# Performance work log

Measured on AMD Instinct MI355X. Metric: run time of the kernel, lower is better.

## Reference

```python
import jax, jax.numpy as jnp
import numpy as np

B, T, V, C = 4, 2048, 1024, 256
NB_L, NB_M, NB_H = 16, 32, 64


def _band_w(basis, coeffs, soft):
    # basis: (V, 2*nb), coeffs: (C, 2*nb) -> w: (V, C)
    w = basis @ coeffs.T
    return jax.nn.softmax(w, axis=0) if soft else w


def _rms_norm(x):
    eps = jnp.asarray(jnp.finfo(x.dtype).eps, x.dtype)
    return x * jax.lax.rsqrt(jnp.mean(jnp.square(x), axis=-1, keepdims=True) + eps)


def _retrieve(x, basis, qc, kc, vc, decay_logit):
    # x: (B,T,V) -> (B,T,C); decay-weighted dense T x T retrieval
    q = x @ _band_w(basis, qc, True)
    k = x @ _band_w(basis, kc, True)
    v = x @ _band_w(basis, vc, True)
    scores = jnp.einsum('btc,bsc->bts', q, k)
    decay = jax.nn.sigmoid(decay_logit)
    pos = jnp.arange(T)
    diff = pos[None, :] - pos[:, None]  # diff[i,j] = j - i (as in torch code)
    dw = (decay ** jnp.maximum(diff - 1, 0).astype(x.dtype)) * (diff > 0).astype(x.dtype)
    return jnp.einsum('bts,bsc->btc', scores * dw[None], v)


def _project(r, basis, oc, out_scale):
    return jnp.einsum('btc,vc->btv', r, basis @ oc.T) * out_scale


def _transform(x, basis, read_c, mix, bias):
    z = x @ _band_w(basis, read_c, True)
    return jax.nn.gelu(z @ mix + bias, approximate=False)


def _write_back(h, basis, write_c, out_scale):
    return jnp.einsum('btc,vc->btv', h, basis @ write_c.T) * out_scale


def setup_inputs() -> dict:
    key = jax.random.key(0)
    ks = iter(jax.random.split(key, 48))
    s = 0.02

    def rn(shape, scale=s):
        return jax.random.normal(next(ks), shape, dtype=jnp.float32) * scale

    d = {
        'x': jax.random.normal(next(ks), (B, T, V), dtype=jnp.float32),
        'basis_low': jax.random.normal(next(ks), (V, 2 * NB_L), dtype=jnp.float32),
        'basis_mid': jax.random.normal(next(ks), (V, 2 * NB_M), dtype=jnp.float32),
        'basis_high': jax.random.normal(next(ks), (V, 2 * NB_H), dtype=jnp.float32),
    }
    for pre, nb, dec in (('slow', NB_L, 4.0), ('fast', NB_H, 2.0)):
        for nm in ('q', 'k', 'v', 'o'):
            d[f'{pre}_{nm}'] = rn((C, 2 * nb))
        d[f'{pre}_decay'] = jnp.asarray(dec, jnp.float32)
        d[f'{pre}_scale'] = jnp.asarray(0.1, jnp.float32)
    for pre, nb in (('low', NB_L), ('mid', NB_M), ('high', NB_H)):
        d[f'{pre}_read'] = rn((C, 2 * nb))
        d[f'{pre}_write'] = rn((C, 2 * nb))
        d[f'{pre}_mix'] = rn((C, C))
        d[f'{pre}_bias'] = jnp.zeros((C,), jnp.float32)
        d[f'{pre}_oscale'] = jnp.asarray(0.1, jnp.float32)
    d['tg_w'] = rn((C, C)); d['tg_b'] = jnp.zeros((C,), jnp.float32)
    d['alpha_w'] = rn((C, C)); d['alpha_b'] = jnp.zeros((C,), jnp.float32)
    for nm in ('mem_slow_scale', 'mem_fast_scale', 'op_low_scale', 'op_mid_scale', 'op_high_scale'):
        d[nm] = jnp.ones((1,), jnp.float32)
    return d


def reference(x, basis_low, basis_mid, basis_high,
              slow_q, slow_k, slow_v, slow_o, slow_decay, slow_scale,
              fast_q, fast_k, fast_v, fast_o, fast_decay, fast_scale,
              low_read, low_write, low_mix, low_bias, low_oscale,
              mid_read, mid_write, mid_mix, mid_bias, mid_oscale,
              high_read, high_write, high_mix, high_bias, high_oscale,
              tg_w, tg_b, alpha_w, alpha_b,
              mem_slow_scale, mem_fast_scale, op_low_scale, op_mid_scale, op_high_scale):
    # Phase 1: temporal mixing
    xn = _rms_norm(x)
    r_slow = _retrieve(xn, basis_low, slow_q, slow_k, slow_v, slow_decay)
    r_fast = _retrieve(xn, basis_high, fast_q, fast_k, fast_v, fast_decay)
    tg = jax.nn.sigmoid(r_slow @ tg_w + tg_b)
    r_fast = tg * r_fast
    x = x + (_project(r_slow, basis_low, slow_o, slow_scale) * mem_slow_scale
             + _project(r_fast, basis_high, fast_o, fast_scale) * mem_fast_scale)
    # Phase 2: band processing
    xn = _rms_norm(x)
    h_low = _transform(xn, basis_low, low_read, low_mix, low_bias)
    h_mid = _transform(xn, basis_mid, mid_read, mid_mix, mid_bias)
    h_high = _transform(xn, basis_high, high_read, high_mix, high_bias)
    ag = jax.nn.sigmoid(h_low @ alpha_w + alpha_b)
    h_high = ag * h_high
    x = x + (_write_back(h_low, basis_low, low_write, low_oscale) * op_low_scale
             + _write_back(h_mid, basis_mid, mid_write, mid_oscale) * op_mid_scale
             + _write_back(h_high, basis_high, high_write, high_oscale) * op_high_scale)
    return x
```

## Files before the change

### kernel.cpp

```cpp
#include <hip/hip_runtime.h>
#include <math.h>

#define BB 4
#define TT 2048
#define VV 1024
#define CC 256
#define MR (BB*TT)

using short8  = __attribute__((ext_vector_type(8))) short;
using ushort8 = __attribute__((ext_vector_type(8))) unsigned short;
using f32x4   = __attribute__((ext_vector_type(4))) float;

__device__ __forceinline__ float bs2f(unsigned short s) {
    return __uint_as_float(((unsigned int)s) << 16);
}
__device__ __forceinline__ unsigned short f2bs(float f) {
    unsigned int u = __float_as_uint(f);
    u += 0x7fffu + ((u >> 16) & 1u);
    return (unsigned short)(u >> 16);
}
__device__ __forceinline__ void gl_lds16(const void* g, void* l) {
    __builtin_amdgcn_global_load_lds(
        (const __attribute__((address_space(1))) unsigned int*)g,
        (__attribute__((address_space(3))) unsigned int*)l, 16, 0, 0);
}
__device__ __forceinline__ float sigm(float x) { return 1.f / (1.f + expf(-x)); }
__device__ __forceinline__ float erf_f(float x) {
    float ax = fabsf(x);
    float t = 1.f / (1.f + 0.3275911f * ax);
    float p = t * (0.254829592f + t * (-0.284496736f + t * (1.421413741f +
              t * (-1.453152027f + t * 1.061405429f))));
    float e = 1.f - p * expf(-ax * ax);
    return copysignf(e, x);
}

struct CastJob { const float* src; unsigned short* dst; int n; };
struct CastArgs { CastJob j[17]; };

__global__ void cast_bf16_multi(CastArgs a) {
    CastJob jb = a.j[blockIdx.x];
    int off = (blockIdx.y * 256 + threadIdx.x) * 8;
    if (off + 8 > jb.n) return;
    float4 v0 = *reinterpret_cast<const float4*>(jb.src + off);
    float4 v1 = *reinterpret_cast<const float4*>(jb.src + off + 4);
    ushort8 u;
    u[0] = f2bs(v0.x); u[1] = f2bs(v0.y); u[2] = f2bs(v0.z); u[3] = f2bs(v0.w);
    u[4] = f2bs(v1.x); u[5] = f2bs(v1.y); u[6] = f2bs(v1.z); u[7] = f2bs(v1.w);
    *reinterpret_cast<ushort8*>(jb.dst + off) = u;
}

__global__ void softmax_rows(unsigned short* __restrict__ w) {
    int row = blockIdx.x * 4 + (threadIdx.x >> 6);
    int lane = threadIdx.x & 63;
    ushort4* rp = reinterpret_cast<ushort4*>(w + (size_t)row * 1024);
    float v[16];
    #pragma unroll
    for (int i = 0; i < 4; ++i) {
        ushort4 u = rp[lane + i * 64];
        v[i*4+0] = bs2f(u.x); v[i*4+1] = bs2f(u.y);
        v[i*4+2] = bs2f(u.z); v[i*4+3] = bs2f(u.w);
    }
    float m = v[0];
    #pragma unroll
    for (int i = 1; i < 16; ++i) m = fmaxf(m, v[i]);
    #pragma unroll
    for (int o = 32; o > 0; o >>= 1) m = fmaxf(m, __shfl_xor(m, o));
    float s = 0.f;
    #pragma unroll
    for (int i = 0; i < 16; ++i) { v[i] = expf(v[i] - m); s += v[i]; }
    #pragma unroll
    for (int o = 32; o > 0; o >>= 1) s += __shfl_xor(s, o);
    float inv = 1.f / s;
    #pragma unroll
    for (int i = 0; i < 4; ++i) {
        ushort4 u;
        u.x = f2bs(v[i*4+0] * inv); u.y = f2bs(v[i*4+1] * inv);
        u.z = f2bs(v[i*4+2] * inv); u.w = f2bs(v[i*4+3] * inv);
        rp[lane + i * 64] = u;
    }
}

__global__ void prep_T5(const float* s0, const float* s1, const float* s2,
                        const float* s3, const float* s4,
                        unsigned short* d0, unsigned short* d1, unsigned short* d2,
                        unsigned short* d3, unsigned short* d4) {
    int y = blockIdx.y;
    const float* W = y == 0 ? s0 : y == 1 ? s1 : y == 2 ? s2 : y == 3 ? s3 : s4;
    unsigned short* WT = y == 0 ? d0 : y == 1 ? d1 : y == 2 ? d2 : y == 3 ? d3 : d4;
    int n = blockIdx.x, k = threadIdx.x;
    WT[(size_t)n * 256 + k] = f2bs(W[(size_t)k * 256 + n]);
}

__global__ void rmsnorm_k(const float* __restrict__ x, unsigned short* __restrict__ xn) {
    int row = blockIdx.x * 4 + (threadIdx.x >> 6);
    int lane = threadIdx.x & 63;
    const float4* src = reinterpret_cast<const float4*>(x + (size_t)row * VV);
    float4 v[4];
    float s = 0.f;
    #pragma unroll
    for (int i = 0; i < 4; ++i) {
        v[i] = src[lane + i * 64];
        s += v[i].x*v[i].x + v[i].y*v[i].y + v[i].z*v[i].z + v[i].w*v[i].w;
    }
    #pragma unroll
    for (int o = 32; o > 0; o >>= 1) s += __shfl_xor(s, o);
    float r = rsqrtf(s * (1.f / VV) + 1.1920929e-7f);
    ushort4* dst = reinterpret_cast<ushort4*>(xn + (size_t)row * VV);
    #pragma unroll
    for (int i = 0; i < 4; ++i) {
        ushort4 u;
        u.x = f2bs(v[i].x * r); u.y = f2bs(v[i].y * r);
        u.z = f2bs(v[i].z * r); u.w = f2bs(v[i].w * r);
        dst[lane + i * 64] = u;
    }
}

__global__ void transpose4_k(const unsigned short* __restrict__ qkv,
                             unsigned short* __restrict__ vt_s,
                             unsigned short* __restrict__ vt_f,
                             unsigned short* __restrict__ kts_s,
                             unsigned short* __restrict__ kts_f,
                             const float* __restrict__ dls,
                             const float* __restrict__ dlf) {
    __shared__ unsigned short tile[32][33];
    int z = blockIdx.z, b = z & 3, which = z >> 2;
    int srcoff = which == 0 ? 512 : which == 1 ? 1280 : which == 2 ? 256 : 1024;
    unsigned short* dst = which == 0 ? vt_s : which == 1 ? vt_f : which == 2 ? kts_s : kts_f;
    float l2d = 0.f;
    if (which == 2) l2d = log2f(sigm(dls[0]));
    if (which == 3) l2d = log2f(sigm(dlf[0]));
    int t0 = blockIdx.x * 32, c0 = blockIdx.y * 32;
    int tx = threadIdx.x & 31, ty = threadIdx.x >> 5;
    const unsigned short* src = qkv + srcoff;
    #pragma unroll
    for (int i = 0; i < 4; ++i) {
        int r = ty + i * 8;
        tile[r][tx] = src[(size_t)(b * TT + t0 + r) * 1536 + c0 + tx];
    }
    __syncthreads();
    float w = (which >= 2) ? exp2f(l2d * (float)((t0 + tx) & 127)) : 1.f;
    #pragma unroll
    for (int i = 0; i < 4; ++i) {
        int r = ty + i * 8;
        dst[((size_t)b * CC + c0 + r) * TT + t0 + tx] = f2bs(bs2f(tile[tx][r]) * w);
    }
}

__device__ __forceinline__ void gemm64_core(
    const unsigned short* A, int lda, const unsigned short* Bt, int ldb,
    int K, int m0, int n0, short8* As, short8* Bs, f32x4 (&acc)[2][2]) {
    const int tid = threadIdx.x;
    const int lane = tid & 63, wid = tid >> 6;
    const int wm = wid >> 1, wn = wid & 1;
    const int lrow = tid >> 2, lch = tid & 3;
    const int sws = lch ^ ((lrow >> 1) & 3);
    const unsigned short* ag = A + (size_t)(m0 + lrow) * lda + lch * 8;
    const unsigned short* bg = Bt + (size_t)(n0 + lrow) * ldb + lch * 8;
    #pragma unroll
    for (int i = 0; i < 2; ++i)
        #pragma unroll
        for (int j = 0; j < 2; ++j) acc[i][j] = {0.f, 0.f, 0.f, 0.f};
    const int g = lane >> 4;
    const int ra0 = wm * 32 + (lane & 15);
    const int rb0 = wn * 32 + (lane & 15);
    for (int k0 = 0; k0 < K; k0 += 32) {
        As[lrow * 4 + sws] = *reinterpret_cast<const short8*>(ag + k0);
        Bs[lrow * 4 + sws] = *reinterpret_cast<const short8*>(bg + k0);
        __syncthreads();
        short8 af[2], bf[2];
        #pragma unroll
        for (int i = 0; i < 2; ++i) {
            int ra = ra0 + i * 16;
            af[i] = As[ra * 4 + (g ^ ((ra >> 1) & 3))];
            int rb = rb0 + i * 16;
            bf[i] = Bs[rb * 4 + (g ^ ((rb >> 1) & 3))];
        }
        #pragma unroll
        for (int i = 0; i < 2; ++i)
            #pragma unroll
            for (int j = 0; j < 2; ++j)
                acc[i][j] = __builtin_amdgcn_mfma_f32_16x16x32_bf16(af[i], bf[j], acc[i][j], 0, 0, 0);
        __syncthreads();
    }
}

#define EPI_LOOP(MV, NV, VV_, BODY)                                            \
    {   const int lane_ = threadIdx.x & 63, wid_ = threadIdx.x >> 6;           \
        const int wm_ = wid_ >> 1, wn_ = wid_ & 1;                             \
        _Pragma("unroll")                                                      \
        for (int i_ = 0; i_ < 2; ++i_)                                         \
        { _Pragma("unroll")                                                    \
          for (int j_ = 0; j_ < 2; ++j_)                                       \
          { _Pragma("unroll")                                                  \
            for (int r_ = 0; r_ < 4; ++r_)                                     \
            { int MV = m0 + wm_ * 32 + i_ * 16 + (lane_ >> 4) * 4 + r_;        \
              int NV = n0 + wn_ * 32 + j_ * 16 + (lane_ & 15);                 \
              float VV_ = acc[i_][j_][r_];                                     \
              BODY } } } }

struct MJob {
    const unsigned short* A; const unsigned short* Bt; unsigned short* outb;
    const float* s1; const float* s2;
    int lda, ldb, K, ldo, gx, nblk;
};
struct MJobs5 { MJob j[5]; };

template<int EPI>
__global__ __launch_bounds__(256)
void gemm_multi_k(MJobs5 js) {
    int bid = blockIdx.x, ji = 0, base = 0;
    while (bid >= base + js.j[ji].nblk) { base += js.j[ji].nblk; ++ji; }
    MJob jb = js.j[ji];
    int rem = bid - base;
    int m0 = (rem / jb.gx) * 64, n0 = (rem % jb.gx) * 64;
    __shared__ short8 As[256], Bs[256];
    f32x4 acc[2][2];
    gemm64_core(jb.A, jb.lda, jb.Bt, jb.ldb, jb.K, m0, n0, As, Bs, acc);
    float sc = 1.f;
    if constexpr (EPI == 4) sc = jb.s1[0] * jb.s2[0];
    EPI_LOOP(m, n, v, { jb.outb[(size_t)m * jb.ldo + n] = f2bs(v * sc); })
}

__global__ __launch_bounds__(256)
void sig_k(const unsigned short* A, int lda, const unsigned short* Bt,
           const float* bias, const unsigned short* aux, int ldaux,
           unsigned short* outb, int ldo, int coloff) {
    int m0 = blockIdx.y * 64, n0 = blockIdx.x * 64;
    __shared__ short8 As[256], Bs[256];
    f32x4 acc[2][2];
    gemm64_core(A, lda, Bt, 256, 256, m0, n0, As, Bs, acc);
    EPI_LOOP(m, n, v, {
        float s = sigm(v + bias[n]);
        float a = bs2f(aux[(size_t)m * ldaux + n]);
        outb[(size_t)m * ldo + coloff + n] = f2bs(s * a);
    })
}

__global__ __launch_bounds__(256)
void gelu3_k(const unsigned short* zbuf, const unsigned short* WT_mix,
             const float* lb, const float* mb, const float* hb,
             unsigned short* hcat, unsigned short* hhigh) {
    int zi = blockIdx.z;
    const unsigned short* A = zbuf + zi * 256;
    const unsigned short* Bt = WT_mix + (size_t)zi * 65536;
    const float* bias = zi == 0 ? lb : zi == 1 ? mb : hb;
    unsigned short* outb = zi == 2 ? hhigh : hcat;
    int ldo = zi == 2 ? 256 : 768;
    int coloff = zi == 1 ? 256 : 0;
    int m0 = blockIdx.y * 64, n0 = blockIdx.x * 64;
    __shared__ short8 As[256], Bs[256];
    f32x4 acc[2][2];
    gemm64_core(A, 768, Bt, 256, 256, m0, n0, As, Bs, acc);
    EPI_LOOP(m, n, v, {
        float z = v + bias[n];
        float h = 0.5f * z * (1.f + erf_f(z * 0.70710678118654752f));
        outb[(size_t)m * ldo + coloff + n] = f2bs(h);
    })
}

__global__ __launch_bounds__(256)
void inter_k(const unsigned short* qkv,
             const unsigned short* ST_s, const unsigned short* ST_f,
             const float* dls, const float* dlf,
             unsigned short* rcat, unsigned short* rfast) {
    int zz = blockIdx.z;
    int sel = zz >= 60, z2 = sel ? zz - 60 : zz;
    int zb = z2 / 15, zp = z2 % 15;
    const unsigned short* A = qkv + (sel ? 768 : 0) + (size_t)(zb * TT + zp * 128) * 1536;
    const unsigned short* Bt = (sel ? ST_f : ST_s) + (size_t)z2 * 65536;
    unsigned short* outb = sel ? rfast : rcat;
    int ldo = sel ? 256 : 512;
    float l2d = log2f(sigm(sel ? dlf[0] : dls[0]));
    int m0 = blockIdx.y * 64, n0 = blockIdx.x * 64;
    __shared__ short8 As[256], Bs[256];
    f32x4 acc[2][2];
    gemm64_core(A, 1536, Bt, 256, 256, m0, n0, As, Bs, acc);
    EPI_LOOP(m, n, v, {
        float rs = exp2f(l2d * (float)(127 - m));
        size_t idx = (size_t)(zb * TT + zp * 128 + m) * ldo + n;
        outb[idx] = f2bs(bs2f(outb[idx]) + v * rs);
    })
}

struct EpiP {
    float* outf; const float* addf;
    unsigned short* outb; int ldo;
    const unsigned short* A2; const unsigned short* B2;
    float* outf2;
};

template<int EPI, int BATCH>
__global__ __launch_bounds__(256)
void gemm128_k(const unsigned short* __restrict__ A, int lda,
               const unsigned short* __restrict__ Bt, int ldb, int K, EpiP ep) {
    __shared__ short8 As[2][512], Bs[2][512];
    const int tid = threadIdx.x;
    const int lane = tid & 63, wid = tid >> 6;
    const int wm = wid >> 1, wn = wid & 1;

    int sel = 0, z2v = 0;
    if constexpr (BATCH == 1) {
        int zz = blockIdx.z; sel = zz >> 6; z2v = zz & 63;
        int zb = z2v >> 4, zp = z2v & 15;
        if (sel) { A = ep.A2; Bt = ep.B2; }
        A  += (size_t)(zb * CC) * lda + zp * 128;
        Bt += (size_t)(zb * CC) * ldb + zp * 128;
    }

    int lin = blockIdx.y * gridDim.x + blockIdx.x;
    int ngw = gridDim.x * gridDim.y;
    int sw = lin;
    if (!(ngw & 7)) sw = (lin & 7) * (ngw >> 3) + (lin >> 3);
    const int m0 = (sw / gridDim.x) * 128, n0 = (sw % gridDim.x) * 128;

    const int srow = lane >> 2, schk = (lane & 3) ^ ((srow >> 1) & 3);
    const unsigned short* ga = A + (size_t)(m0 + wid * 32 + srow) * lda + schk * 8;
    const unsigned short* gb = Bt + (size_t)(n0 + wid * 32 + srow) * ldb + schk * 8;

    const int fr = lane & 15, fg = lane >> 4;

    f32x4 acc[4][4];
    #pragma unroll
    for (int i = 0; i < 4; ++i)
        #pragma unroll
        for (int j = 0; j < 4; ++j) acc[i][j] = {0.f, 0.f, 0.f, 0.f};

    auto stage = [&](int buf, int k0) {
        short8* lA = &As[buf][(wid * 32) * 4];
        short8* lB = &Bs[buf][(wid * 32) * 4];
        gl_lds16(ga + k0, lA);
        gl_lds16(ga + (size_t)16 * lda + k0, lA + 64);
        gl_lds16(gb + k0, lB);
        gl_lds16(gb + (size_t)16 * ldb + k0, lB + 64);
    };

    stage(0, 0);
    int cur = 0;
    for (int k0 = 0; k0 < K; k0 += 32) {
        if (k0 + 32 < K) {
            stage(cur ^ 1, k0 + 32);
            asm volatile("s_waitcnt vmcnt(4)" ::: "memory");
        } else {
            asm volatile("s_waitcnt vmcnt(0)" ::: "memory");
        }
        __builtin_amdgcn_s_barrier();
        __builtin_amdgcn_sched_barrier(0);
        short8 af[4], bf[4];
        #pragma unroll
        for (int i = 0; i < 4; ++i) {
            int ra = wm * 64 + i * 16 + fr;
            af[i] = As[cur][ra * 4 + (fg ^ ((ra >> 1) & 3))];
            int rb = wn * 64 + i * 16 + fr;
            bf[i] = Bs[cur][rb * 4 + (fg ^ ((rb >> 1) & 3))];
        }
        #pragma unroll
        for (int i = 0; i < 4; ++i)
            #pragma unroll
            for (int j = 0; j < 4; ++j)
                acc[i][j] = __builtin_amdgcn_mfma_f32_16x16x32_bf16(af[i], bf[j], acc[i][j], 0, 0, 0);
        __builtin_amdgcn_sched_barrier(0);
        __builtin_amdgcn_s_barrier();
        cur ^= 1;
    }

    float* gout = nullptr;
    if constexpr (EPI == 5) gout = (sel ? ep.outf2 : ep.outf) + (size_t)z2v * 65536;

    #pragma unroll
    for (int i = 0; i < 4; ++i) {
        #pragma unroll
        for (int j = 0; j < 4; ++j) {
            #pragma unroll
            for (int r = 0; r < 4; ++r) {
                int m = m0 + wm * 64 + i * 16 + fg * 4 + r;
                int n = n0 + wn * 64 + j * 16 + fr;
                float v = acc[i][j][r];
                if constexpr (EPI == 0) {
                    ep.outb[(size_t)m * ep.ldo + n] = f2bs(v);
                } else if constexpr (EPI == 3) {
                    size_t idx = (size_t)m * ep.ldo + n;
                    ep.outf[idx] = ep.addf[idx] + v;
                } else {
                    gout[(size_t)m * 256 + n] = v;
                }
            }
        }
    }
}

__global__ __launch_bounds__(256)
void attn_k(const unsigned short* __restrict__ qkv,
            const unsigned short* __restrict__ vt_s,
            const unsigned short* __restrict__ vt_f,
            const float* __restrict__ dls, const float* __restrict__ dlf,
            unsigned short* __restrict__ rcat, unsigned short* __restrict__ rfast) {
    int y = blockIdx.y;
    int qoff = y ? 768 : 0, koff = y ? 1024 : 256;
    const unsigned short* vt = y ? vt_f : vt_s;
    unsigned short* rout = y ? rfast : rcat;
    int ldr = y ? 256 : 512;
    float l2d = log2f(sigm(y ? dlf[0] : dls[0]));

    int blk = blockIdx.x;
    int b = blk >> 7;
    int t0 = (blk & 127) << 4;
    int tid = threadIdx.x;
    int lane = tid & 63, wid = tid >> 6;

    __shared__ short8 Pl[4][64];
    __shared__ float  red[16][260];

    short8 qf[8];
    const size_t rowq = (size_t)(b * TT + t0 + (lane & 15)) * 1536 + qoff + (lane >> 4) * 8;
    #pragma unroll
    for (int ch = 0; ch < 8; ++ch)
        qf[ch] = *reinterpret_cast<const short8*>(qkv + rowq + ch * 32);

    f32x4 racc[16];
    #pragma unroll
    for (int i = 0; i < 16; ++i) racc[i] = {0.f, 0.f, 0.f, 0.f};

    unsigned short* pb = reinterpret_cast<unsigned short*>(&Pl[wid][0]);

    int sBeg = t0 & ~31;
    int sEnd = (t0 & ~127) + 128;
    const int tl = (lane >> 4) * 4;

    for (int s0 = sBeg + wid * 32; s0 < sEnd; s0 += 128) {
        #pragma unroll
        for (int h = 0; h < 2; ++h) {
            f32x4 sacc = {0.f, 0.f, 0.f, 0.f};
            const unsigned short* kb =
                qkv + (size_t)(b * TT + s0 + h * 16 + (lane & 15)) * 1536 + koff + (lane >> 4) * 8;
            #pragma unroll
            for (int ch = 0; ch < 8; ++ch) {
                short8 kf = *reinterpret_cast<const short8*>(kb + ch * 32);
                sacc = __builtin_amdgcn_mfma_f32_16x16x32_bf16(qf[ch], kf, sacc, 0, 0, 0);
            }
            int scol = s0 + h * 16 + (lane & 15);
            #pragma unroll
            for (int r = 0; r < 4; ++r) {
                int trow = t0 + tl + r;
                int d = scol - trow;
                float w = (d > 0) ? exp2f(l2d * (float)(d - 1)) : 0.f;
                int prow = tl + r, pcol = h * 16 + (lane & 15);
                int swp = (pcol >> 3) ^ ((prow >> 1) & 3);
                pb[(prow * 4 + swp) * 8 + (pcol & 7)] = f2bs(sacc[r] * w);
            }
        }
        asm volatile("s_waitcnt lgkmcnt(0)" ::: "memory");
        __builtin_amdgcn_sched_barrier(0);
        short8 pf;
        { int prow = lane & 15; pf = Pl[wid][prow * 4 + ((lane >> 4) ^ ((prow >> 1) & 3))]; }
        const unsigned short* vb = vt + ((size_t)b * CC + (lane & 15)) * TT + s0 + (lane >> 4) * 8;
        #pragma unroll
        for (int nt = 0; nt < 16; ++nt) {
            short8 vf = *reinterpret_cast<const short8*>(vb + (size_t)nt * 16 * TT);
            racc[nt] = __builtin_amdgcn_mfma_f32_16x16x32_bf16(pf, vf, racc[nt], 0, 0, 0);
        }
    }

    for (int w = 0; w < 4; ++w) {
        if (wid == w) {
            #pragma unroll
            for (int nt = 0; nt < 16; ++nt)
                #pragma unroll
                for (int r = 0; r < 4; ++r) {
                    int row = tl + r, col = nt * 16 + (lane & 15);
                    if (w == 0) red[row][col] = racc[nt][r];
                    else        red[row][col] += racc[nt][r];
                }
        }
        __syncthreads();
    }

    {
        int row = tid >> 4, c0 = (tid & 15) * 16;
        ushort8 lo, hi;
        #pragma unroll
        for (int j = 0; j < 8; ++j) lo[j] = f2bs(red[row][c0 + j]);
        #pragma unroll
        for (int j = 0; j < 8; ++j) hi[j] = f2bs(red[row][c0 + 8 + j]);
        unsigned short* dst = rout + (size_t)(b * TT + t0 + row) * ldr + c0;
        *reinterpret_cast<ushort8*>(dst)     = lo;
        *reinterpret_cast<ushort8*>(dst + 8) = hi;
    }
}

__global__ void scan_states2(const float* __restrict__ Gs, const float* __restrict__ Gf,
                             const float* __restrict__ dls, const float* __restrict__ dlf,
                             unsigned short* __restrict__ STs, unsigned short* __restrict__ STf) {
    int sel = blockIdx.z;
    const float* G = sel ? Gf : Gs;
    unsigned short* ST = sel ? STf : STs;
    float d = sigm(sel ? dlf[0] : dls[0]);
    int b = blockIdx.y;
    int e0 = (blockIdx.x * 256 + threadIdx.x) * 4;
    float dL = exp2f(log2f(d) * 128.f);
    float4 s = {0.f, 0.f, 0.f, 0.f};
    for (int c = 15; c >= 1; --c) {
        float4 g = *reinterpret_cast<const float4*>(G + (((size_t)(b * 16 + c)) << 16) + e0);
        s.x = g.x + dL * s.x; s.y = g.y + dL * s.y;
        s.z = g.z + dL * s.z; s.w = g.w + dL * s.w;
        ushort4 o;
        o.x = f2bs(s.x); o.y = f2bs(s.y); o.z = f2bs(s.z); o.w = f2bs(s.w);
        *reinterpret_cast<ushort4*>(ST + (((size_t)(b * 15 + c - 1)) << 16) + e0) = o;
    }
}

extern "C" void kernel_launch(void* const* d_in, const int* in_sizes, int n_in,
                              void* d_out, int out_size, void* d_ws, size_t ws_size,
                              hipStream_t stream) {
    (void)in_sizes; (void)n_in; (void)out_size; (void)ws_size;
    const float* x          = (const float*)d_in[0];
    const float* basis_low  = (const float*)d_in[1];
    const float* basis_mid  = (const float*)d_in[2];
    const float* basis_high = (const float*)d_in[3];
    const float* slow_q = (const float*)d_in[4];
    const float* slow_k = (const float*)d_in[5];
    const float* slow_v = (const float*)d_in[6];
    const float* slow_o = (const float*)d_in[7];
    const float* slow_decay = (const float*)d_in[8];
    const float* slow_scale = (const float*)d_in[9];
    const float* fast_q = (const float*)d_in[10];
    const float* fast_k = (const float*)d_in[11];
    const float* fast_v = (const float*)d_in[12];
    const float* fast_o = (const float*)d_in[13];
    const float* fast_decay = (const float*)d_in[14];
    const float* fast_scale = (const float*)d_in[15];
    const float* low_read  = (const float*)d_in[16];
    const float* low_write = (const float*)d_in[17];
    const float* low_mix   = (const float*)d_in[18];
    const float* low_bias  = (const float*)d_in[19];
    const float* low_oscale= (const float*)d_in[20];
    const float* mid_read  = (const float*)d_in[21];
    const float* mid_write = (const float*)d_in[22];
    const float* mid_mix   = (const float*)d_in[23];
    const float* mid_bias  = (const float*)d_in[24];
    const float* mid_oscale= (const float*)d_in[25];
    const float* high_read  = (const float*)d_in[26];
    const float* high_write = (const float*)d_in[27];
    const float* high_mix   = (const float*)d_in[28];
    const float* high_bias  = (const float*)d_in[29];
    const float* high_oscale= (const float*)d_in[30];
    const float* tg_w    = (const float*)d_in[31];
    const float* tg_b    = (const float*)d_in[32];
    const float* alpha_w = (const float*)d_in[33];
    const float* alpha_b = (const float*)d_in[34];
    const float* mem_slow_scale = (const float*)d_in[35];
    const float* mem_fast_scale = (const float*)d_in[36];
    const float* op_low_scale   = (const float*)d_in[37];
    const float* op_mid_scale   = (const float*)d_in[38];
    const float* op_high_scale  = (const float*)d_in[39];
    float* out = (float*)d_out;

    char* ws = (char*)d_ws;
    size_t off = 0;
    auto alloc = [&](size_t n) { char* p = ws + off; off += (n + 255) & ~(size_t)255; return p; };
    unsigned short* WT_p1   = (unsigned short*)alloc((size_t)6 * CC * VV * 2);
    unsigned short* WT_read = (unsigned short*)alloc((size_t)3 * CC * VV * 2);
    unsigned short* Wcat_o  = (unsigned short*)alloc((size_t)VV * 512 * 2);
    unsigned short* Wcat_w  = (unsigned short*)alloc((size_t)VV * 768 * 2);
    unsigned short* WT_mix  = (unsigned short*)alloc((size_t)3 * 65536 * 2);
    unsigned short* WT_tg   = (unsigned short*)alloc((size_t)65536 * 2);
    unsigned short* WT_al   = (unsigned short*)alloc((size_t)65536 * 2);
    unsigned short* bb_low  = (unsigned short*)alloc((size_t)VV * 32 * 2);
    unsigned short* bb_mid  = (unsigned short*)alloc((size_t)VV * 64 * 2);
    unsigned short* bb_high = (unsigned short*)alloc((size_t)VV * 128 * 2);
    unsigned short* cqkv_l  = (unsigned short*)alloc((size_t)768 * 32 * 2);
    unsigned short* cqkv_h  = (unsigned short*)alloc((size_t)768 * 128 * 2);
    unsigned short* crd_l   = (unsigned short*)alloc((size_t)256 * 32 * 2);
    unsigned short* crd_m   = (unsigned short*)alloc((size_t)256 * 64 * 2);
    unsigned short* crd_h   = (unsigned short*)alloc((size_t)256 * 128 * 2);
    unsigned short* cO_s    = (unsigned short*)alloc((size_t)256 * 32 * 2);
    unsigned short* cO_f    = (unsigned short*)alloc((size_t)256 * 128 * 2);
    unsigned short* cW_l    = (unsigned short*)alloc((size_t)256 * 32 * 2);
    unsigned short* cW_m    = (unsigned short*)alloc((size_t)256 * 64 * 2);
    unsigned short* cW_h    = (unsigned short*)alloc((size_t)256 * 128 * 2);
    unsigned short* xn      = (unsigned short*)alloc((size_t)MR * VV * 2);
    unsigned short* qkv     = (unsigned short*)alloc((size_t)MR * 1536 * 2);
    unsigned short* vt_s    = (unsigned short*)alloc((size_t)BB * CC * TT * 2);
    unsigned short* vt_f    = (unsigned short*)alloc((size_t)BB * CC * TT * 2);
    unsigned short* kts_s   = (unsigned short*)alloc((size_t)BB * CC * TT * 2);
    unsigned short* kts_f   = (unsigned short*)alloc((size_t)BB * CC * TT * 2);
    unsigned short* ST_s    = (unsigned short*)alloc((size_t)BB * 15 * 65536 * 2);
    unsigned short* ST_f    = (unsigned short*)alloc((size_t)BB * 15 * 65536 * 2);
    unsigned short* rcat    = (unsigned short*)alloc((size_t)MR * 512 * 2);
    unsigned short* rfast   = (unsigned short*)alloc((size_t)MR * CC * 2);
    unsigned short* hhigh   = (unsigned short*)alloc((size_t)MR * CC * 2);
    float* Gs = (float*)xn;
    float* Gf = (float*)rcat;
    unsigned short* z    = qkv;
    unsigned short* hcat = qkv + (size_t)MR * 768;

    {
        CastArgs ca;
        int i = 0;
        auto J = [&](const float* s, unsigned short* d, int n) { ca.j[i].src = s; ca.j[i].dst = d; ca.j[i].n = n; ++i; };
        J(basis_low,  bb_low,  VV * 32);
        J(basis_mid,  bb_mid,  VV * 64);
        J(basis_high, bb_high, VV * 128);
        J(slow_q, cqkv_l + 0 * 256 * 32, 256 * 32);
        J(slow_k, cqkv_l + 1 * 256 * 32, 256 * 32);
        J(slow_v, cqkv_l + 2 * 256 * 32, 256 * 32);
        J(fast_q, cqkv_h + 0 * 256 * 128, 256 * 128);
        J(fast_k, cqkv_h + 1 * 256 * 128, 256 * 128);
        J(fast_v, cqkv_h + 2 * 256 * 128, 256 * 128);
        J(low_read,  crd_l, 256 * 32);
        J(mid_read,  crd_m, 256 * 64);
        J(high_read, crd_h, 256 * 128);
        J(slow_o,    cO_s,  256 * 32);
        J(fast_o,    cO_f,  256 * 128);
        J(low_write, cW_l,  256 * 32);
        J(mid_write, cW_m,  256 * 64);
        J(high_write,cW_h,  256 * 128);
        cast_bf16_multi<<<dim3(17, 64), 256, 0, stream>>>(ca);
    }

    {
        MJobs5 js;
        auto S = [&](int i, const unsigned short* A, int lda, const unsigned short* B, int K,
                     unsigned short* o, int nb) {
            js.j[i].A = A; js.j[i].Bt = B; js.j[i].outb = o; js.j[i].s1 = nullptr; js.j[i].s2 = nullptr;
            js.j[i].lda = lda; js.j[i].ldb = K; js.j[i].K = K; js.j[i].ldo = VV; js.j[i].gx = 16; js.j[i].nblk = nb;
        };
        S(0, cqkv_l, 32,  bb_low,  32,  WT_p1,                    192);
        S(1, cqkv_h, 128, bb_high, 128, WT_p1 + (size_t)768 * VV, 192);
        S(2, crd_l,  32,  bb_low,  32,  WT_read,                   64);
        S(3, crd_m,  64,  bb_mid,  64,  WT_read + (size_t)256 * VV, 64);
        S(4, crd_h,  128, bb_high, 128, WT_read + (size_t)512 * VV, 64);
        gemm_multi_k<0><<<576, 256, 0, stream>>>(js);
    }
    softmax_rows<<<576, 256, 0, stream>>>(WT_p1);

    {
        MJobs5 js;
        auto S = [&](int i, const unsigned short* A, int lda, const unsigned short* B, int K,
                     unsigned short* o, int ldo, const float* s1, const float* s2) {
            js.j[i].A = A; js.j[i].Bt = B; js.j[i].outb = o; js.j[i].s1 = s1; js.j[i].s2 = s2;
            js.j[i].lda = lda; js.j[i].ldb = K; js.j[i].K = K; js.j[i].ldo = ldo; js.j[i].gx = 4; js.j[i].nblk = 64;
        };
        S(0, bb_low,  32,  cO_s, 32,  Wcat_o,       512, slow_scale,  mem_slow_scale);
        S(1, bb_high, 128, cO_f, 128, Wcat_o + 256, 512, fast_scale,  mem_fast_scale);
        S(2, bb_low,  32,  cW_l, 32,  Wcat_w,       768, low_oscale,  op_low_scale);
        S(3, bb_mid,  64,  cW_m, 64,  Wcat_w + 256, 768, mid_oscale,  op_mid_scale);
        S(4, bb_high, 128, cW_h, 128, Wcat_w + 512, 768, high_oscale, op_high_scale);
        gemm_multi_k<4><<<320, 256, 0, stream>>>(js);
    }

    prep_T5<<<dim3(256, 5), 256, 0, stream>>>(tg_w, alpha_w, low_mix, mid_mix, high_mix,
                                              WT_tg, WT_al, WT_mix, WT_mix + 65536, WT_mix + 131072);

    rmsnorm_k<<<MR / 4, 256, 0, stream>>>(x, xn);
    { EpiP ep{}; ep.outb = qkv; ep.ldo = 1536;
      gemm128_k<0,0><<<dim3(12, 64), 256, 0, stream>>>(xn, 1024, WT_p1, 1024, 1024, ep); }
    transpose4_k<<<dim3(64, 8, 16), 256, 0, stream>>>(qkv, vt_s, vt_f, kts_s, kts_f, slow_decay, fast_decay);
    { EpiP ep{}; ep.outf = Gs; ep.outf2 = Gf; ep.A2 = vt_f; ep.B2 = kts_f;
      gemm128_k<5,1><<<dim3(2, 2, 128), 256, 0, stream>>>(vt_s, TT, kts_s, TT, 128, ep); }
    scan_states2<<<dim3(64, 4, 2), 256, 0, stream>>>(Gs, Gf, slow_decay, fast_decay, ST_s, ST_f);
    attn_k<<<dim3(512, 2), 256, 0, stream>>>(qkv, vt_s, vt_f, slow_decay, fast_decay, rcat, rfast);
    inter_k<<<dim3(4, 2, 120), 256, 0, stream>>>(qkv, ST_s, ST_f, slow_decay, fast_decay, rcat, rfast);
    sig_k<<<dim3(4, 128), 256, 0, stream>>>(rcat, 512, WT_tg, tg_b, rfast, 256, rcat, 512, 256);
    { EpiP ep{}; ep.outf = out; ep.addf = x; ep.ldo = 1024;
      gemm128_k<3,0><<<dim3(8, 64), 256, 0, stream>>>(rcat, 512, Wcat_o, 512, 512, ep); }

    rmsnorm_k<<<MR / 4, 256, 0, stream>>>(out, xn);
    { EpiP ep{}; ep.outb = z; ep.ldo = 768;
      gemm128_k<0,0><<<dim3(6, 64), 256, 0, stream>>>(xn, 1024, WT_read, 1024, 1024, ep); }
    gelu3_k<<<dim3(4, 128, 3), 256, 0, stream>>>(z, WT_mix, low_bias, mid_bias, high_bias, hcat, hhigh);
    sig_k<<<dim3(4, 128), 256, 0, stream>>>(hcat, 768, WT_al, alpha_b, hhigh, 256, hcat, 768, 512);
    { EpiP ep{}; ep.outf = out; ep.addf = out; ep.ldo = 1024;
      gemm128_k<3,0><<<dim3(6, 64), 256, 0, stream>>>(hcat, 768, Wcat_w, 768, 768, ep); }
}
```

Before: 277.6 us.

## Widen gemm128 K-step to 64 and fold inter-chunk kernel into it

Replaces the double-buffered K=32 main loop of the shared 128x128 GEMM with a single-buffered K=64 step using an 8-chunk XOR swizzle and plain __syncthreads. The separate 64x64 inter_k kernel is removed and its work moves into a new batched gemm128 epilogue that scales by the decay factor and accumulates into the bf16 outputs. The larger K step halves barrier count per tile but drops the load/compute overlap that double buffering gave. Every GEMM in the pipeline is affected, and the inter-chunk launch now uses far fewer blocks (240 instead of 960).

```diff
diff --git a/kernel.cpp b/kernel.cpp
--- a/kernel.cpp
+++ b/kernel.cpp
@@ -258,53 +258,37 @@
     })
 }
 
-__global__ __launch_bounds__(256)
-void inter_k(const unsigned short* qkv,
-             const unsigned short* ST_s, const unsigned short* ST_f,
-             const float* dls, const float* dlf,
-             unsigned short* rcat, unsigned short* rfast) {
-    int zz = blockIdx.z;
-    int sel = zz >= 60, z2 = sel ? zz - 60 : zz;
-    int zb = z2 / 15, zp = z2 % 15;
-    const unsigned short* A = qkv + (sel ? 768 : 0) + (size_t)(zb * TT + zp * 128) * 1536;
-    const unsigned short* Bt = (sel ? ST_f : ST_s) + (size_t)z2 * 65536;
-    unsigned short* outb = sel ? rfast : rcat;
-    int ldo = sel ? 256 : 512;
-    float l2d = log2f(sigm(sel ? dlf[0] : dls[0]));
-    int m0 = blockIdx.y * 64, n0 = blockIdx.x * 64;
-    __shared__ short8 As[256], Bs[256];
-    f32x4 acc[2][2];
-    gemm64_core(A, 1536, Bt, 256, 256, m0, n0, As, Bs, acc);
-    EPI_LOOP(m, n, v, {
-        float rs = exp2f(l2d * (float)(127 - m));
-        size_t idx = (size_t)(zb * TT + zp * 128 + m) * ldo + n;
-        outb[idx] = f2bs(bs2f(outb[idx]) + v * rs);
-    })
-}
-
 struct EpiP {
     float* outf; const float* addf;
     unsigned short* outb; int ldo;
     const unsigned short* A2; const unsigned short* B2;
     float* outf2;
+    unsigned short* outb2; int ldo2;
+    const float* dls; const float* dlf;
 };
 
 template<int EPI, int BATCH>
 __global__ __launch_bounds__(256)
 void gemm128_k(const unsigned short* __restrict__ A, int lda,
                const unsigned short* __restrict__ Bt, int ldb, int K, EpiP ep) {
-    __shared__ short8 As[2][512], Bs[2][512];
+    __shared__ short8 As[1024], Bs[1024];
     const int tid = threadIdx.x;
     const int lane = tid & 63, wid = tid >> 6;
     const int wm = wid >> 1, wn = wid & 1;
 
-    int sel = 0, z2v = 0;
+    int sel = 0, z2v = 0, zb = 0, zp = 0;
     if constexpr (BATCH == 1) {
         int zz = blockIdx.z; sel = zz >> 6; z2v = zz & 63;
-        int zb = z2v >> 4, zp = z2v & 15;
+        zb = z2v >> 4; zp = z2v & 15;
         if (sel) { A = ep.A2; Bt = ep.B2; }
         A  += (size_t)(zb * CC) * lda + zp * 128;
         Bt += (size_t)(zb * CC) * ldb + zp * 128;
+    } else if constexpr (BATCH == 2) {
+        int zz = blockIdx.z; sel = zz >= 60 ? 1 : 0; z2v = sel ? zz - 60 : zz;
+        zb = z2v / 15; zp = z2v % 15;
+        if (sel) Bt = ep.B2;
+        A  += (sel ? 768 : 0) + (size_t)(zb * TT + zp * 128) * lda;
+        Bt += (size_t)z2v * 65536;
     }
 
     int lin = blockIdx.y * gridDim.x + blockIdx.x;
@@ -313,9 +297,11 @@
     if (!(ngw & 7)) sw = (lin & 7) * (ngw >> 3) + (lin >> 3);
     const int m0 = (sw / gridDim.x) * 128, n0 = (sw % gridDim.x) * 128;
 
-    const int srow = lane >> 2, schk = (lane & 3) ^ ((srow >> 1) & 3);
+    const int srow = lane >> 3, schk = (lane & 7) ^ srow;
     const unsigned short* ga = A + (size_t)(m0 + wid * 32 + srow) * lda + schk * 8;
     const unsigned short* gb = Bt + (size_t)(n0 + wid * 32 + srow) * ldb + schk * 8;
+    short8* lA = &As[(wid * 32) * 8];
+    short8* lB = &Bs[(wid * 32) * 8];
 
     const int fr = lane & 15, fg = lane >> 4;
 
@@ -325,44 +311,37 @@
         #pragma unroll
         for (int j = 0; j < 4; ++j) acc[i][j] = {0.f, 0.f, 0.f, 0.f};
 
-    auto stage = [&](int buf, int k0) {
-        short8* lA = &As[buf][(wid * 32) * 4];
-        short8* lB = &Bs[buf][(wid * 32) * 4];
-        gl_lds16(ga + k0, lA);
-        gl_lds16(ga + (size_t)16 * lda + k0, lA + 64);
-        gl_lds16(gb + k0, lB);
-        gl_lds16(gb + (size_t)16 * ldb + k0, lB + 64);
-    };
-
-    stage(0, 0);
-    int cur = 0;
-    for (int k0 = 0; k0 < K; k0 += 32) {
-        if (k0 + 32 < K) {
-            stage(cur ^ 1, k0 + 32);
-            asm volatile("s_waitcnt vmcnt(4)" ::: "memory");
-        } else {
-            asm volatile("s_waitcnt vmcnt(0)" ::: "memory");
+    for (int k0 = 0; k0 < K; k0 += 64) {
+        #pragma unroll
+        for (int q = 0; q < 4; ++q) {
+            gl_lds16(ga + (size_t)(q * 8) * lda + k0, lA + q * 64);
+            gl_lds16(gb + (size_t)(q * 8) * ldb + k0, lB + q * 64);
         }
-        __builtin_amdgcn_s_barrier();
-        __builtin_amdgcn_sched_barrier(0);
-        short8 af[4], bf[4];
-        #pragma unroll
-        for (int i = 0; i < 4; ++i) {
-            int ra = wm * 64 + i * 16 + fr;
-            af[i] = As[cur][ra * 4 + (fg ^ ((ra >> 1) & 3))];
-            int rb = wn * 64 + i * 16 + fr;
-            bf[i] = Bs[cur][rb * 4 + (fg ^ ((rb >> 1) & 3))];
+        __syncthreads();
+        #pragma unroll
+        for (int kk = 0; kk < 2; ++kk) {
+            short8 af[4], bf[4];
+            #pragma unroll
+            for (int i = 0; i < 4; ++i) {
+                int ra = wm * 64 + i * 16 + fr;
+                af[i] = As[ra * 8 + ((kk * 4 + fg) ^ (ra & 7))];
+                int rb = wn * 64 + i * 16 + fr;
+                bf[i] = Bs[rb * 8 + ((kk * 4 + fg) ^ (rb & 7))];
+            }
+            #pragma unroll
+            for (int i = 0; i < 4; ++i)
+                #pragma unroll
+                for (int j = 0; j < 4; ++j)
+                    acc[i][j] = __builtin_amdgcn_mfma_f32_16x16x32_bf16(af[i], bf[j], acc[i][j], 0, 0, 0);
         }
-        #pragma unroll
-        for (int i = 0; i < 4; ++i)
-            #pragma unroll
-            for (int j = 0; j < 4; ++j)
-                acc[i][j] = __builtin_amdgcn_mfma_f32_16x16x32_bf16(af[i], bf[j], acc[i][j], 0, 0, 0);
-        __builtin_amdgcn_sched_barrier(0);
-        __builtin_amdgcn_s_barrier();
-        cur ^= 1;
-    }
-
+        __syncthreads();
+    }
+
+    float l2d6 = 0.f;
+    if constexpr (EPI == 6) l2d6 = log2f(sigm(sel ? ep.dlf[0] : ep.dls[0]));
+    unsigned short* ob = ep.outb;
+    int ldo = ep.ldo;
+    if constexpr (EPI == 6) { if (sel) { ob = ep.outb2; ldo = ep.ldo2; } }
     float* gout = nullptr;
     if constexpr (EPI == 5) gout = (sel ? ep.outf2 : ep.outf) + (size_t)z2v * 65536;
 
@@ -376,12 +355,16 @@
                 int n = n0 + wn * 64 + j * 16 + fr;
                 float v = acc[i][j][r];
                 if constexpr (EPI == 0) {
-                    ep.outb[(size_t)m * ep.ldo + n] = f2bs(v);
+                    ob[(size_t)m * ldo + n] = f2bs(v);
                 } else if constexpr (EPI == 3) {
                     size_t idx = (size_t)m * ep.ldo + n;
                     ep.outf[idx] = ep.addf[idx] + v;
-                } else {
+                } else if constexpr (EPI == 5) {
                     gout[(size_t)m * 256 + n] = v;
+                } else if constexpr (EPI == 6) {
+                    float rs = exp2f(l2d6 * (float)(127 - m));
+                    size_t idx = (size_t)(zb * TT + zp * 128 + m) * ldo + n;
+                    ob[idx] = f2bs(bs2f(ob[idx]) + v * rs);
                 }
             }
         }
@@ -659,7 +642,9 @@
       gemm128_k<5,1><<<dim3(2, 2, 128), 256, 0, stream>>>(vt_s, TT, kts_s, TT, 128, ep); }
     scan_states2<<<dim3(64, 4, 2), 256, 0, stream>>>(Gs, Gf, slow_decay, fast_decay, ST_s, ST_f);
     attn_k<<<dim3(512, 2), 256, 0, stream>>>(qkv, vt_s, vt_f, slow_decay, fast_decay, rcat, rfast);
-    inter_k<<<dim3(4, 2, 120), 256, 0, stream>>>(qkv, ST_s, ST_f, slow_decay, fast_decay, rcat, rfast);
+    { EpiP ep{}; ep.outb = rcat; ep.ldo = 512; ep.outb2 = rfast; ep.ldo2 = 256;
+      ep.dls = slow_decay; ep.dlf = fast_decay; ep.B2 = ST_f;
+      gemm128_k<6,2><<<dim3(2, 1, 120), 256, 0, stream>>>(qkv, 1536, ST_s, 256, 256, ep); }
     sig_k<<<dim3(4, 128), 256, 0, stream>>>(rcat, 512, WT_tg, tg_b, rfast, 256, rcat, 512, 256);
     { EpiP ep{}; ep.outf = out; ep.addf = x; ep.ldo = 1024;
       gemm128_k<3,0><<<dim3(8, 64), 256, 0, stream>>>(rcat, 512, Wcat_o, 512, 512, ep); }
```

New measurement: 274.8 us. Within noise of the previous version (-1.0%).
